# Optimization experiments

Measured on AMD Instinct MI355X. Metric: run time of the kernel, lower is better.

## Reference

```python
import jax, jax.numpy as jnp
import numpy as np

T, S, B, H, E, I = 64, 400, 32, 512, 1024, 128


def setup_inputs() -> dict:
    key = jax.random.key(0)
    ks = jax.random.split(key, 16)
    def n(k, shape, scale=1.0):
        return jax.random.normal(k, shape, dtype=jnp.float32) * scale
    return {
        "embedded_y": n(ks[0], (T, B, I)),
        "encode_outputs": n(ks[1], (S, B, E)),
        "init_state": n(ks[2], (B, H)),
        "x_mask": jnp.ones((S, B, 1), jnp.float32),
        "y_mask": jnp.ones((T, B, 1), jnp.float32),
        "x_index": jax.random.randint(ks[3], (S, B), 0, 50000, dtype=jnp.int32),
        "init_coverage": jnp.zeros((B, S), jnp.float32),
        # attention params
        "W_h": n(ks[4], (E, E), E ** -0.5),
        "W_s": n(ks[5], (E, H), H ** -0.5),
        "W_c": n(ks[6], (E, 1), 1.0),
        "b_attn": n(ks[7], (E,), 0.02),
        "V": n(ks[8], (1, E), E ** -0.5),
        # gru1: input I -> hidden H (torch gate order r, z, n)
        "w_ih1": n(ks[9], (3 * H, I), I ** -0.5),
        "w_hh1": n(ks[10], (3 * H, H), H ** -0.5),
        "b_ih1": jnp.zeros((3 * H,), jnp.float32),
        "b_hh1": jnp.zeros((3 * H,), jnp.float32),
        # gru2: input E(=2H) -> hidden H
        "w_ih2": n(ks[11], (3 * H, E), E ** -0.5),
        "w_hh2": n(ks[12], (3 * H, H), H ** -0.5),
        "b_ih2": jnp.zeros((3 * H,), jnp.float32),
        "b_hh2": jnp.zeros((3 * H,), jnp.float32),
    }


def _gru_cell(x, h, w_ih, w_hh, b_ih, b_hh):
    # single-step nn.GRU (torch gate order: r, z, n)
    gi = x @ w_ih.T + b_ih
    gh = h @ w_hh.T + b_hh
    i_r, i_z, i_n = jnp.split(gi, 3, axis=-1)
    h_r, h_z, h_n = jnp.split(gh, 3, axis=-1)
    r = jax.nn.sigmoid(i_r + h_r)
    z = jax.nn.sigmoid(i_z + h_z)
    n_ = jnp.tanh(i_n + r * h_n)
    return (1.0 - z) * n_ + z * h


def reference(embedded_y, encode_outputs, init_state, x_mask, y_mask, x_index,
              init_coverage, W_h, W_s, W_c, b_attn, V,
              w_ih1, w_hh1, b_ih1, b_hh1, w_ih2, w_hh2, b_ih2, b_hh2):
    # hoist the encoder projection out of the time loop (loop-invariant)
    Wh_enc = jnp.einsum('sbe,fe->sbf', encode_outputs, W_h)  # [S,B,E]
    wc = W_c[:, 0]  # [E], since W_c: Linear(1, E)

    def step(carry, inp):
        hidden, cov = carry          # [B,H], [B,S]
        y_t, ym = inp                # [B,I], [B,1]
        s1 = _gru_cell(y_t, hidden, w_ih1, w_hh1, b_ih1, b_hh1)
        s1 = ym * s1 + (1.0 - ym) * hidden
        # Bahdanau attention with coverage
        states = Wh_enc + (s1 @ W_s.T)[None, :, :] + cov.T[:, :, None] * wc + b_attn  # [S,B,E]
        score = (jnp.tanh(states) * x_mask) @ V.T            # [S,B,1]
        score = jnp.where(x_mask == 0, -1e9, score)
        aw = jax.nn.softmax(score, axis=0)                   # softmax over source positions
        ctx = jnp.sum(aw * encode_outputs, axis=0)           # [B,E]
        s2 = _gru_cell(ctx, s1, w_ih2, w_hh2, b_ih2, b_hh2)
        s2 = ym * s2 + (1.0 - ym) * s1
        wa = aw[:, :, 0].T                                   # [B,S]
        return (s2, cov + wa), (s2, ctx, wa, cov)

    _, (hidden_states, context_vectors, words_attention_weights, coverage_vectors) = \
        jax.lax.scan(step, (init_state, init_coverage), (embedded_y, y_mask))
    Tn = embedded_y.shape[0]
    x_index_t = x_index.T  # [B,S]
    x_indexes = jnp.broadcast_to(x_index_t[None], (Tn,) + x_index_t.shape)
    # is_predicting=False: coverage BEFORE each step (coverage_vectors_all[:-1])
    return (hidden_states, context_vectors, words_attention_weights, x_indexes, coverage_vectors)
```

## Files before the change

kernel.cpp:

```cpp
#include <hip/hip_runtime.h>
#include <cstdint>
#include <cstddef>

#define T_ 64
#define S_ 400
#define B_ 32
#define H_ 512
#define E_ 1024
#define I_ 128

__device__ __forceinline__ float sigmoid_(float x){ return 1.0f/(1.0f + __expf(-x)); }
__device__ __forceinline__ float tanh_(float x){
    float e = __expf(2.0f*fabsf(x));
    float t = 1.0f - 2.0f/(e + 1.0f);
    return copysignf(t, x);
}


__global__ __launch_bounds__(256) void init_kernel(const float* __restrict__ init_state,
        const float* __restrict__ init_cov, float* __restrict__ h0, float* __restrict__ cov){
    int i = blockIdx.x*256 + threadIdx.x;
    if (i < B_*H_) h0[i] = init_state[i];
    if (i < B_*S_) cov[i] = init_cov[i];
}

__global__ __launch_bounds__(256) void xidx_kernel(const int* __restrict__ x_index, float* __restrict__ out){
    int i = blockIdx.x*256 + threadIdx.x;
    if (i >= T_*B_*S_) return;
    int s = i % S_;
    int b = (i / S_) % B_;
    out[i] = (float)x_index[s*B_ + b];
}

#define BM 64
#define BN 64
#define BK 16
__global__ __launch_bounds__(256) void gemm_whenc(const float* __restrict__ A,
        const float* __restrict__ Bw, float* __restrict__ C){
    __shared__ float As[BK][BM];
    __shared__ float Bs[BK][BN];
    int bm = blockIdx.x;
    int bn = blockIdx.y;
    int tid = threadIdx.x;
    int lrow  = tid >> 2;
    int lcol4 = (tid & 3) * 4;
    int tx = tid & 15, ty = tid >> 4;
    const float* Ab = A  + (size_t)(bm*BM)*1024;
    const float* Bb = Bw + (size_t)(bn*BN)*1024;
    float acc[4][4] = {};
    for (int k0 = 0; k0 < 1024; k0 += BK){
        float4 av = *(const float4*)(Ab + (size_t)lrow*1024 + k0 + lcol4);
        float4 bv = *(const float4*)(Bb + (size_t)lrow*1024 + k0 + lcol4);
        As[lcol4+0][lrow]=av.x; As[lcol4+1][lrow]=av.y; As[lcol4+2][lrow]=av.z; As[lcol4+3][lrow]=av.w;
        Bs[lcol4+0][lrow]=bv.x; Bs[lcol4+1][lrow]=bv.y; Bs[lcol4+2][lrow]=bv.z; Bs[lcol4+3][lrow]=bv.w;
        __syncthreads();
        #pragma unroll
        for (int kk = 0; kk < BK; ++kk){
            float4 a4 = *(const float4*)&As[kk][ty*4];
            float4 b4 = *(const float4*)&Bs[kk][tx*4];
            float a_[4] = {a4.x, a4.y, a4.z, a4.w};
            float b_[4] = {b4.x, b4.y, b4.z, b4.w};
            #pragma unroll
            for (int i=0;i<4;++i)
                #pragma unroll
                for (int j=0;j<4;++j) acc[i][j] = fmaf(a_[i], b_[j], acc[i][j]);
        }
        __syncthreads();
    }
    int m0 = bm*BM + ty*4, n0 = bn*BN + tx*4;
    #pragma unroll
    for (int i=0;i<4;++i){
        float4 o = make_float4(acc[i][0], acc[i][1], acc[i][2], acc[i][3]);
        *(float4*)&C[(size_t)(m0+i)*E_ + n0] = o;
    }
}


__global__ __launch_bounds__(256) void gru1_kernel(const float* __restrict__ y,
        const float* __restrict__ hid,
        const float* __restrict__ w_ih, const float* __restrict__ w_hh,
        const float* __restrict__ b_ih, const float* __restrict__ b_hh,
        const float* __restrict__ ymask, float* __restrict__ s1, int t){
    __shared__ float xs[I_];
    __shared__ float hs[H_];
    __shared__ float part[3][64][6];
    int tid = threadIdx.x;
    int b = blockIdx.y;
    int hh = tid & 63, p = tid >> 6;
    int h = blockIdx.x*64 + hh;
    for (int i=tid; i<I_; i+=256) xs[i] = y[(size_t)t*B_*I_ + (size_t)b*I_ + i];
    for (int i=tid; i<H_; i+=256) hs[i] = hid[(size_t)b*H_ + i];
    __syncthreads();
    float gp[6];
    #pragma unroll
    for (int g=0; g<3; ++g){
        const float* wr = w_ih + (size_t)(g*H_ + h)*I_;
        float acc = 0.0f;
        for (int k = p*32; k < p*32 + 32; k += 4){
            float4 w4 = *(const float4*)(wr + k);
            acc = fmaf(w4.x, xs[k+0], acc); acc = fmaf(w4.y, xs[k+1], acc);
            acc = fmaf(w4.z, xs[k+2], acc); acc = fmaf(w4.w, xs[k+3], acc);
        }
        gp[g] = acc;
    }
    #pragma unroll
    for (int g=0; g<3; ++g){
        const float* wr = w_hh + (size_t)(g*H_ + h)*H_;
        float acc = 0.0f;
        for (int k = p*128; k < p*128 + 128; k += 4){
            float4 w4 = *(const float4*)(wr + k);
            acc = fmaf(w4.x, hs[k+0], acc); acc = fmaf(w4.y, hs[k+1], acc);
            acc = fmaf(w4.z, hs[k+2], acc); acc = fmaf(w4.w, hs[k+3], acc);
        }
        gp[3+g] = acc;
    }
    if (p){ 
        #pragma unroll
        for (int j=0;j<6;++j) part[p-1][hh][j] = gp[j]; 
    }
    __syncthreads();
    if (p == 0){
        float gi[3], gh[3];
        #pragma unroll
        for (int j=0;j<3;++j) gi[j] = gp[j]   + part[0][hh][j]   + part[1][hh][j]   + part[2][hh][j]   + b_ih[j*H_ + h];
        #pragma unroll
        for (int j=0;j<3;++j) gh[j] = gp[3+j] + part[0][hh][3+j] + part[1][hh][3+j] + part[2][hh][3+j] + b_hh[j*H_ + h];
        float r = sigmoid_(gi[0] + gh[0]);
        float z = sigmoid_(gi[1] + gh[1]);
        float n = tanh_(gi[2] + r*gh[2]);
        float hv = hs[h];
        float sv = (1.0f - z)*n + z*hv;
        float ym = ymask[t*B_ + b];
        s1[(size_t)b*H_ + h] = ym*sv + (1.0f - ym)*hv;
    }
}

__global__ __launch_bounds__(256) void qproj_kernel(const float* __restrict__ s1,
        const float* __restrict__ W_s, const float* __restrict__ b_attn, float* __restrict__ qb){
    __shared__ float hs[H_];
    __shared__ float part[3][64];
    int tid = threadIdx.x;
    int b = blockIdx.y;
    int ff = tid & 63, p = tid >> 6;
    int f = blockIdx.x*64 + ff;
    for (int i=tid; i<H_; i+=256) hs[i] = s1[(size_t)b*H_ + i];
    __syncthreads();
    const float* wr = W_s + (size_t)f*H_;
    float acc = 0.0f;
    for (int k = p*128; k < p*128 + 128; k += 4){
        float4 w4 = *(const float4*)(wr + k);
        acc = fmaf(w4.x, hs[k+0], acc); acc = fmaf(w4.y, hs[k+1], acc);
        acc = fmaf(w4.z, hs[k+2], acc); acc = fmaf(w4.w, hs[k+3], acc);
    }
    if (p) part[p-1][ff] = acc;
    __syncthreads();
    if (p == 0) qb[(size_t)b*E_ + f] = acc + part[0][ff] + part[1][ff] + part[2][ff] + b_attn[f];
}

__global__ __launch_bounds__(256) void score_kernel(const float* __restrict__ whenc,
        const float* __restrict__ qb, const float* __restrict__ cov,
        const float* __restrict__ wc, const float* __restrict__ Vv,
        const float* __restrict__ xmask, float* __restrict__ scores_t){
    int wave = blockIdx.x*4 + (threadIdx.x >> 6);
    int lane = threadIdx.x & 63;
    int s = wave >> 5, b = wave & 31;
    const float* wp = whenc + (size_t)(s*B_ + b)*E_;
    const float* qp = qb + (size_t)b*E_;
    float cv = cov[b*S_ + s];
    float acc = 0.0f;
    #pragma unroll
    for (int i=0;i<4;++i){
        int e = (i*64 + lane)*4;
        float4 w4 = *(const float4*)(wp + e);
        float4 q4 = *(const float4*)(qp + e);
        float4 c4 = *(const float4*)(wc + e);
        float4 v4 = *(const float4*)(Vv + e);
        acc = fmaf(v4.x, tanh_(w4.x + q4.x + cv*c4.x), acc);
        acc = fmaf(v4.y, tanh_(w4.y + q4.y + cv*c4.y), acc);
        acc = fmaf(v4.z, tanh_(w4.z + q4.z + cv*c4.z), acc);
        acc = fmaf(v4.w, tanh_(w4.w + q4.w + cv*c4.w), acc);
    }
    #pragma unroll
    for (int off=32; off; off>>=1) acc += __shfl_xor(acc, off);
    if (lane == 0){
        float xm = xmask[s*B_ + b];
        scores_t[b*S_ + s] = (xm == 0.0f) ? -1e9f : acc*xm;
    }
}

__global__ __launch_bounds__(256) void ctx_kernel(const float* __restrict__ scores_t,
        const float* __restrict__ enc, float* __restrict__ cov, float* __restrict__ ctxbuf,
        float* __restrict__ out_ctx, float* __restrict__ out_wa, float* __restrict__ out_cov, int t){
    __shared__ float p[S_];
    __shared__ float sacc[4][64];
    __shared__ float red[8];
    int tid = threadIdx.x;
    int b  = blockIdx.y;
    int e0 = blockIdx.x * 64;
    float v0 = scores_t[b*S_ + tid];
    float v1 = (tid + 256 < S_) ? scores_t[b*S_ + tid + 256] : -1e30f;
    float mx = fmaxf(v0, v1);
    #pragma unroll
    for (int off=32; off; off>>=1) mx = fmaxf(mx, __shfl_xor(mx, off));
    int wid = tid >> 6, lane = tid & 63;
    if (lane == 0) red[wid] = mx;
    __syncthreads();
    mx = fmaxf(fmaxf(red[0], red[1]), fmaxf(red[2], red[3]));
    float e0v = __expf(v0 - mx);
    float e1v = (tid + 256 < S_) ? __expf(v1 - mx) : 0.0f;
    float sm = e0v + e1v;
    #pragma unroll
    for (int off=32; off; off>>=1) sm += __shfl_xor(sm, off);
    if (lane == 0) red[4 + wid] = sm;
    __syncthreads();
    float rden = 1.0f/(red[4] + red[5] + red[6] + red[7]);
    p[tid] = e0v * rden;
    if (tid + 256 < S_) p[tid + 256] = e1v * rden;
    __syncthreads();
    const float* ep = enc + (size_t)b*E_ + e0 + lane;
    float acc = 0.0f;
    int sbeg = wid*100, send = sbeg + 100;
    #pragma unroll 4
    for (int s = sbeg; s < send; ++s)
        acc = fmaf(p[s], ep[(size_t)s*(B_*E_)], acc);
    sacc[wid][lane] = acc;
    __syncthreads();
    if (wid == 0){
        float a = sacc[0][lane] + sacc[1][lane] + sacc[2][lane] + sacc[3][lane];
        int e = e0 + lane;
        ctxbuf[(size_t)b*E_ + e] = a;
        out_ctx[(size_t)t*B_*E_ + (size_t)b*E_ + e] = a;
    }
    if (blockIdx.x == 0){
        for (int s = tid; s < S_; s += 256){
            float c = cov[b*S_ + s];
            out_wa [(size_t)t*B_*S_ + (size_t)b*S_ + s] = p[s];
            out_cov[(size_t)t*B_*S_ + (size_t)b*S_ + s] = c;
            cov[b*S_ + s] = c + p[s];
        }
    }
}

__global__ __launch_bounds__(256) void gru2_kernel(const float* __restrict__ ctx,
        const float* __restrict__ s1,
        const float* __restrict__ w_ih, const float* __restrict__ w_hh,
        const float* __restrict__ b_ih, const float* __restrict__ b_hh,
        const float* __restrict__ ymask, float* __restrict__ hnext,
        float* __restrict__ out_hidden, int t){
    __shared__ float xs[E_];
    __shared__ float hs[H_];
    __shared__ float part[3][64][6];
    int tid = threadIdx.x;
    int b = blockIdx.y;
    int hh = tid & 63, p = tid >> 6;
    int h = blockIdx.x*64 + hh;
    for (int i=tid; i<E_; i+=256) xs[i] = ctx[(size_t)b*E_ + i];
    for (int i=tid; i<H_; i+=256) hs[i] = s1[(size_t)b*H_ + i];
    __syncthreads();
    float gp[6];
    #pragma unroll
    for (int g=0; g<3; ++g){
        const float* wr = w_ih + (size_t)(g*H_ + h)*E_;
        float acc = 0.0f;
        for (int k = p*256; k < p*256 + 256; k += 4){
            float4 w4 = *(const float4*)(wr + k);
            acc = fmaf(w4.x, xs[k+0], acc); acc = fmaf(w4.y, xs[k+1], acc);
            acc = fmaf(w4.z, xs[k+2], acc); acc = fmaf(w4.w, xs[k+3], acc);
        }
        gp[g] = acc;
    }
    #pragma unroll
    for (int g=0; g<3; ++g){
        const float* wr = w_hh + (size_t)(g*H_ + h)*H_;
        float acc = 0.0f;
        for (int k = p*128; k < p*128 + 128; k += 4){
            float4 w4 = *(const float4*)(wr + k);
            acc = fmaf(w4.x, hs[k+0], acc); acc = fmaf(w4.y, hs[k+1], acc);
            acc = fmaf(w4.z, hs[k+2], acc); acc = fmaf(w4.w, hs[k+3], acc);
        }
        gp[3+g] = acc;
    }
    if (p){ 
        #pragma unroll
        for (int j=0;j<6;++j) part[p-1][hh][j] = gp[j]; 
    }
    __syncthreads();
    if (p == 0){
        float gi[3], gh[3];
        #pragma unroll
        for (int j=0;j<3;++j) gi[j] = gp[j]   + part[0][hh][j]   + part[1][hh][j]   + part[2][hh][j]   + b_ih[j*H_ + h];
        #pragma unroll
        for (int j=0;j<3;++j) gh[j] = gp[3+j] + part[0][hh][3+j] + part[1][hh][3+j] + part[2][hh][3+j] + b_hh[j*H_ + h];
        float r = sigmoid_(gi[0] + gh[0]);
        float z = sigmoid_(gi[1] + gh[1]);
        float n = tanh_(gi[2] + r*gh[2]);
        float s1v = hs[h];
        float sv = (1.0f - z)*n + z*s1v;
        float ym = ymask[t*B_ + b];
        float o = ym*sv + (1.0f - ym)*s1v;
        hnext[(size_t)b*H_ + h] = o;
        out_hidden[(size_t)t*B_*H_ + (size_t)b*H_ + h] = o;
    }
}


extern "C" void kernel_launch(void* const* d_in, const int* in_sizes, int n_in,
                              void* d_out, int out_size, void* d_ws, size_t ws_size,
                              hipStream_t stream) {
    const float* y          = (const float*)d_in[0];
    const float* enc        = (const float*)d_in[1];
    const float* init_state = (const float*)d_in[2];
    const float* xmask      = (const float*)d_in[3];
    const float* ymask      = (const float*)d_in[4];
    const int*   x_index    = (const int*)  d_in[5];
    const float* init_cov   = (const float*)d_in[6];
    const float* W_h        = (const float*)d_in[7];
    const float* W_s        = (const float*)d_in[8];
    const float* W_c        = (const float*)d_in[9];
    const float* b_attn     = (const float*)d_in[10];
    const float* Vv         = (const float*)d_in[11];
    const float* w_ih1      = (const float*)d_in[12];
    const float* w_hh1      = (const float*)d_in[13];
    const float* b_ih1      = (const float*)d_in[14];
    const float* b_hh1      = (const float*)d_in[15];
    const float* w_ih2      = (const float*)d_in[16];
    const float* w_hh2      = (const float*)d_in[17];
    const float* b_ih2      = (const float*)d_in[18];
    const float* b_hh2      = (const float*)d_in[19];

    float* out        = (float*)d_out;
    float* out_hidden = out;
    float* out_ctx    = out_hidden + (size_t)T_*B_*H_;
    float* out_wa     = out_ctx    + (size_t)T_*B_*E_;
    float* out_xidx   = out_wa     + (size_t)T_*B_*S_;
    float* out_cov    = out_xidx   + (size_t)T_*B_*S_;

    float* ws     = (float*)d_ws;
    float* whenc  = ws;
    float* qb     = whenc  + (size_t)S_*B_*E_;
    float* s1     = qb     + (size_t)B_*E_;
    float* h0     = s1     + (size_t)B_*H_;
    float* h1     = h0     + (size_t)B_*H_;
    float* cov    = h1     + (size_t)B_*H_;
    float* scores = cov    + (size_t)B_*S_;
    float* ctxbuf = scores + (size_t)B_*S_;

    init_kernel<<<64, 256, 0, stream>>>(init_state, init_cov, h0, cov);
    xidx_kernel<<<3200, 256, 0, stream>>>(x_index, out_xidx);
    gemm_whenc<<<dim3(200, 16), 256, 0, stream>>>(enc, W_h, whenc);

    for (int t = 0; t < T_; ++t){
        float* hcur  = (t & 1) ? h1 : h0;
        float* hnext = (t & 1) ? h0 : h1;
        gru1_kernel<<<dim3(8, 32), 256, 0, stream>>>(y, hcur, w_ih1, w_hh1, b_ih1, b_hh1, ymask, s1, t);
        qproj_kernel<<<dim3(16, 32), 256, 0, stream>>>(s1, W_s, b_attn, qb);
        score_kernel<<<3200, 256, 0, stream>>>(whenc, qb, cov, W_c, Vv, xmask, scores);
        ctx_kernel<<<dim3(16, 32), 256, 0, stream>>>(scores, enc, cov, ctxbuf, out_ctx, out_wa, out_cov, t);
        gru2_kernel<<<dim3(8, 32), 256, 0, stream>>>(ctxbuf, s1, w_ih2, w_hh2, b_ih2, b_hh2, ymask, hnext, out_hidden, t);
    }
}
```

Measured before the change: 7.281 ms.

## Fuse per-timestep decoder kernels into one persistent cooperative kernel with grid syncs

Replaces the five per-timestep kernel launches (gru1, qproj, score, ctx, gru2) with one cooperative persistent kernel of 256 blocks that loops over all timesteps and separates phases with grid.sync. Each block keeps its slice of the recurrent weights, W_s rows, W_c and V in LDS across timesteps. The goal is to remove launch overhead and repeated weight reloads. The trade-off is one block per CU, which leaves the bandwidth-heavy score and context phases at low occupancy, plus five grid-wide barriers per step.

```diff
diff --git a/kernel.cpp b/kernel.cpp
--- a/kernel.cpp
+++ b/kernel.cpp
@@ -1,6 +1,9 @@
 #include <hip/hip_runtime.h>
+#include <hip/hip_cooperative_groups.h>
 #include <cstdint>
 #include <cstddef>
+
+namespace cg = cooperative_groups;
 
 #define T_ 64
 #define S_ 400
@@ -15,13 +18,17 @@
     float t = 1.0f - 2.0f/(e + 1.0f);
     return copysignf(t, x);
 }
+__device__ __forceinline__ void fma4_(float& acc, float4 a, float4 b){
+    acc = fmaf(a.x,b.x,acc); acc = fmaf(a.y,b.y,acc);
+    acc = fmaf(a.z,b.z,acc); acc = fmaf(a.w,b.w,acc);
+}
 
 
 __global__ __launch_bounds__(256) void init_kernel(const float* __restrict__ init_state,
-        const float* __restrict__ init_cov, float* __restrict__ h0, float* __restrict__ cov){
+        const float* __restrict__ init_cov, float* __restrict__ h_g, float* __restrict__ covg){
     int i = blockIdx.x*256 + threadIdx.x;
-    if (i < B_*H_) h0[i] = init_state[i];
-    if (i < B_*S_) cov[i] = init_cov[i];
+    if (i < B_*H_) h_g[i] = init_state[i];
+    if (i < B_*S_) covg[i] = init_cov[i];
 }
 
 __global__ __launch_bounds__(256) void xidx_kernel(const int* __restrict__ x_index, float* __restrict__ out){
@@ -76,230 +83,239 @@
 }
 
 
-__global__ __launch_bounds__(256) void gru1_kernel(const float* __restrict__ y,
-        const float* __restrict__ hid,
-        const float* __restrict__ w_ih, const float* __restrict__ w_hh,
+struct PArgs {
+    const float *y, *enc, *xmask, *ymask, *whenc;
+    const float *w_ih1, *w_hh1, *b_ih1, *b_hh1;
+    const float *w_ih2, *w_hh2, *b_ih2, *b_hh2;
+    const float *W_s, *b_attn, *W_c, *V;
+    float *s1g, *qbg, *h_g, *covg, *scoresg;
+    float *out_hidden, *out_ctx, *out_wa, *out_cov;
+};
+
+template<int XDIM, bool WIH_LDS>
+__device__ __forceinline__ void gru_phase(int bid, int tid, int t,
+        const float* __restrict__ xsrc,
+        const float* __restrict__ hsrc,
+        const float* __restrict__ wih,
+        const float* __restrict__ whh_l,
         const float* __restrict__ b_ih, const float* __restrict__ b_hh,
-        const float* __restrict__ ymask, float* __restrict__ s1, int t){
-    __shared__ float xs[I_];
-    __shared__ float hs[H_];
-    __shared__ float part[3][64][6];
-    int tid = threadIdx.x;
-    int b = blockIdx.y;
-    int hh = tid & 63, p = tid >> 6;
-    int h = blockIdx.x*64 + hh;
-    for (int i=tid; i<I_; i+=256) xs[i] = y[(size_t)t*B_*I_ + (size_t)b*I_ + i];
-    for (int i=tid; i<H_; i+=256) hs[i] = hid[(size_t)b*H_ + i];
-    __syncthreads();
-    float gp[6];
+        const float* __restrict__ ymask,
+        float* __restrict__ dest, float* __restrict__ dest2)
+{
+    constexpr int XSEG = XDIM/8;
+    int b = tid >> 3, seg = tid & 7;
+    const float* xb = xsrc + (size_t)b*XDIM + seg*XSEG;
+    const float* hb = hsrc + (size_t)b*H_ + seg*64;
+    float acc[12];
+    #pragma unroll
+    for (int j=0;j<12;++j) acc[j]=0.f;
     #pragma unroll
     for (int g=0; g<3; ++g){
-        const float* wr = w_ih + (size_t)(g*H_ + h)*I_;
-        float acc = 0.0f;
-        for (int k = p*32; k < p*32 + 32; k += 4){
-            float4 w4 = *(const float4*)(wr + k);
-            acc = fmaf(w4.x, xs[k+0], acc); acc = fmaf(w4.y, xs[k+1], acc);
-            acc = fmaf(w4.z, xs[k+2], acc); acc = fmaf(w4.w, xs[k+3], acc);
-        }
-        gp[g] = acc;
+        const float* wr0;
+        const float* wr1;
+        if (WIH_LDS){
+            wr0 = wih + (g*2+0)*XDIM + seg*XSEG;
+            wr1 = wih + (g*2+1)*XDIM + seg*XSEG;
+        } else {
+            wr0 = wih + (size_t)(g*H_ + 2*bid + 0)*XDIM + seg*XSEG;
+            wr1 = wih + (size_t)(g*H_ + 2*bid + 1)*XDIM + seg*XSEG;
+        }
+        #pragma unroll 4
+        for (int k=0; k<XSEG; k+=4){
+            float4 xv = *(const float4*)(xb + k);
+            fma4_(acc[g*2+0], xv, *(const float4*)(wr0 + k));
+            fma4_(acc[g*2+1], xv, *(const float4*)(wr1 + k));
+        }
+        const float* hr0 = whh_l + (g*2+0)*H_ + seg*64;
+        const float* hr1 = whh_l + (g*2+1)*H_ + seg*64;
+        #pragma unroll 4
+        for (int k=0; k<64; k+=4){
+            float4 hv = *(const float4*)(hb + k);
+            fma4_(acc[6+g*2+0], hv, *(const float4*)(hr0 + k));
+            fma4_(acc[6+g*2+1], hv, *(const float4*)(hr1 + k));
+        }
     }
     #pragma unroll
-    for (int g=0; g<3; ++g){
-        const float* wr = w_hh + (size_t)(g*H_ + h)*H_;
-        float acc = 0.0f;
-        for (int k = p*128; k < p*128 + 128; k += 4){
-            float4 w4 = *(const float4*)(wr + k);
-            acc = fmaf(w4.x, hs[k+0], acc); acc = fmaf(w4.y, hs[k+1], acc);
-            acc = fmaf(w4.z, hs[k+2], acc); acc = fmaf(w4.w, hs[k+3], acc);
-        }
-        gp[3+g] = acc;
-    }
-    if (p){ 
+    for (int j=0;j<12;++j){
+        acc[j] += __shfl_xor(acc[j], 1);
+        acc[j] += __shfl_xor(acc[j], 2);
+        acc[j] += __shfl_xor(acc[j], 4);
+    }
+    if (seg == 0){
+        float ym = ymask[t*B_ + b];
         #pragma unroll
-        for (int j=0;j<6;++j) part[p-1][hh][j] = gp[j]; 
+        for (int hh=0; hh<2; ++hh){
+            int h = 2*bid + hh;
+            float gi_r = acc[0+hh] + b_ih[0*H_ + h];
+            float gi_z = acc[2+hh] + b_ih[1*H_ + h];
+            float gi_n = acc[4+hh] + b_ih[2*H_ + h];
+            float gh_r = acc[6+0+hh] + b_hh[0*H_ + h];
+            float gh_z = acc[6+2+hh] + b_hh[1*H_ + h];
+            float gh_n = acc[6+4+hh] + b_hh[2*H_ + h];
+            float r = sigmoid_(gi_r + gh_r);
+            float z = sigmoid_(gi_z + gh_z);
+            float n = tanh_(gi_n + r*gh_n);
+            float hv = hsrc[(size_t)b*H_ + h];
+            float o = ym*((1.f - z)*n + z*hv) + (1.f - ym)*hv;
+            dest[(size_t)b*H_ + h] = o;
+            if (dest2) dest2[(size_t)b*H_ + h] = o;
+        }
+    }
+}
+
+__global__ __launch_bounds__(256, 1) void decoder_persistent(PArgs a){
+    cg::grid_group grid = cg::this_grid();
+    extern __shared__ float smem[];
+    float* wih1_l = smem;
+    float* whh1_l = wih1_l + 6*I_;
+    float* whh2_l = whh1_l + 6*H_;
+    float* wsr    = whh2_l + 6*H_;
+    float* wc_l   = wsr + 4*H_;
+    float* v_l    = wc_l + E_;
+    float* ps     = v_l + E_;
+    float* tmp    = ps + S_;
+    float* red    = tmp + 128;
+
+    const int tid = threadIdx.x;
+    const int bid = blockIdx.x;
+
+    for (int i = tid; i < 6*I_; i += 256){
+        int j = i >> 7, k = i & (I_-1);
+        int g = j >> 1, hh = j & 1;
+        wih1_l[i] = a.w_ih1[(size_t)(g*H_ + 2*bid + hh)*I_ + k];
+    }
+    for (int i = tid; i < 6*H_; i += 256){
+        int j = i >> 9, k = i & (H_-1);
+        int g = j >> 1, hh = j & 1;
+        whh1_l[i] = a.w_hh1[(size_t)(g*H_ + 2*bid + hh)*H_ + k];
+        whh2_l[i] = a.w_hh2[(size_t)(g*H_ + 2*bid + hh)*H_ + k];
+    }
+    for (int i = tid; i < 4*H_; i += 256){
+        int j = i >> 9, k = i & (H_-1);
+        wsr[i] = a.W_s[(size_t)(4*bid + j)*H_ + k];
+    }
+    for (int i = tid; i < E_; i += 256){
+        wc_l[i] = a.W_c[i];
+        v_l[i]  = a.V[i];
     }
     __syncthreads();
-    if (p == 0){
-        float gi[3], gh[3];
-        #pragma unroll
-        for (int j=0;j<3;++j) gi[j] = gp[j]   + part[0][hh][j]   + part[1][hh][j]   + part[2][hh][j]   + b_ih[j*H_ + h];
-        #pragma unroll
-        for (int j=0;j<3;++j) gh[j] = gp[3+j] + part[0][hh][3+j] + part[1][hh][3+j] + part[2][hh][3+j] + b_hh[j*H_ + h];
-        float r = sigmoid_(gi[0] + gh[0]);
-        float z = sigmoid_(gi[1] + gh[1]);
-        float n = tanh_(gi[2] + r*gh[2]);
-        float hv = hs[h];
-        float sv = (1.0f - z)*n + z*hv;
-        float ym = ymask[t*B_ + b];
-        s1[(size_t)b*H_ + h] = ym*sv + (1.0f - ym)*hv;
-    }
-}
-
-__global__ __launch_bounds__(256) void qproj_kernel(const float* __restrict__ s1,
-        const float* __restrict__ W_s, const float* __restrict__ b_attn, float* __restrict__ qb){
-    __shared__ float hs[H_];
-    __shared__ float part[3][64];
-    int tid = threadIdx.x;
-    int b = blockIdx.y;
-    int ff = tid & 63, p = tid >> 6;
-    int f = blockIdx.x*64 + ff;
-    for (int i=tid; i<H_; i+=256) hs[i] = s1[(size_t)b*H_ + i];
-    __syncthreads();
-    const float* wr = W_s + (size_t)f*H_;
-    float acc = 0.0f;
-    for (int k = p*128; k < p*128 + 128; k += 4){
-        float4 w4 = *(const float4*)(wr + k);
-        acc = fmaf(w4.x, hs[k+0], acc); acc = fmaf(w4.y, hs[k+1], acc);
-        acc = fmaf(w4.z, hs[k+2], acc); acc = fmaf(w4.w, hs[k+3], acc);
-    }
-    if (p) part[p-1][ff] = acc;
-    __syncthreads();
-    if (p == 0) qb[(size_t)b*E_ + f] = acc + part[0][ff] + part[1][ff] + part[2][ff] + b_attn[f];
-}
-
-__global__ __launch_bounds__(256) void score_kernel(const float* __restrict__ whenc,
-        const float* __restrict__ qb, const float* __restrict__ cov,
-        const float* __restrict__ wc, const float* __restrict__ Vv,
-        const float* __restrict__ xmask, float* __restrict__ scores_t){
-    int wave = blockIdx.x*4 + (threadIdx.x >> 6);
-    int lane = threadIdx.x & 63;
-    int s = wave >> 5, b = wave & 31;
-    const float* wp = whenc + (size_t)(s*B_ + b)*E_;
-    const float* qp = qb + (size_t)b*E_;
-    float cv = cov[b*S_ + s];
-    float acc = 0.0f;
-    #pragma unroll
-    for (int i=0;i<4;++i){
-        int e = (i*64 + lane)*4;
-        float4 w4 = *(const float4*)(wp + e);
-        float4 q4 = *(const float4*)(qp + e);
-        float4 c4 = *(const float4*)(wc + e);
-        float4 v4 = *(const float4*)(Vv + e);
-        acc = fmaf(v4.x, tanh_(w4.x + q4.x + cv*c4.x), acc);
-        acc = fmaf(v4.y, tanh_(w4.y + q4.y + cv*c4.y), acc);
-        acc = fmaf(v4.z, tanh_(w4.z + q4.z + cv*c4.z), acc);
-        acc = fmaf(v4.w, tanh_(w4.w + q4.w + cv*c4.w), acc);
-    }
-    #pragma unroll
-    for (int off=32; off; off>>=1) acc += __shfl_xor(acc, off);
-    if (lane == 0){
-        float xm = xmask[s*B_ + b];
-        scores_t[b*S_ + s] = (xm == 0.0f) ? -1e9f : acc*xm;
-    }
-}
-
-__global__ __launch_bounds__(256) void ctx_kernel(const float* __restrict__ scores_t,
-        const float* __restrict__ enc, float* __restrict__ cov, float* __restrict__ ctxbuf,
-        float* __restrict__ out_ctx, float* __restrict__ out_wa, float* __restrict__ out_cov, int t){
-    __shared__ float p[S_];
-    __shared__ float sacc[4][64];
-    __shared__ float red[8];
-    int tid = threadIdx.x;
-    int b  = blockIdx.y;
-    int e0 = blockIdx.x * 64;
-    float v0 = scores_t[b*S_ + tid];
-    float v1 = (tid + 256 < S_) ? scores_t[b*S_ + tid + 256] : -1e30f;
-    float mx = fmaxf(v0, v1);
-    #pragma unroll
-    for (int off=32; off; off>>=1) mx = fmaxf(mx, __shfl_xor(mx, off));
-    int wid = tid >> 6, lane = tid & 63;
-    if (lane == 0) red[wid] = mx;
-    __syncthreads();
-    mx = fmaxf(fmaxf(red[0], red[1]), fmaxf(red[2], red[3]));
-    float e0v = __expf(v0 - mx);
-    float e1v = (tid + 256 < S_) ? __expf(v1 - mx) : 0.0f;
-    float sm = e0v + e1v;
-    #pragma unroll
-    for (int off=32; off; off>>=1) sm += __shfl_xor(sm, off);
-    if (lane == 0) red[4 + wid] = sm;
-    __syncthreads();
-    float rden = 1.0f/(red[4] + red[5] + red[6] + red[7]);
-    p[tid] = e0v * rden;
-    if (tid + 256 < S_) p[tid + 256] = e1v * rden;
-    __syncthreads();
-    const float* ep = enc + (size_t)b*E_ + e0 + lane;
-    float acc = 0.0f;
-    int sbeg = wid*100, send = sbeg + 100;
-    #pragma unroll 4
-    for (int s = sbeg; s < send; ++s)
-        acc = fmaf(p[s], ep[(size_t)s*(B_*E_)], acc);
-    sacc[wid][lane] = acc;
-    __syncthreads();
-    if (wid == 0){
-        float a = sacc[0][lane] + sacc[1][lane] + sacc[2][lane] + sacc[3][lane];
-        int e = e0 + lane;
-        ctxbuf[(size_t)b*E_ + e] = a;
-        out_ctx[(size_t)t*B_*E_ + (size_t)b*E_ + e] = a;
-    }
-    if (blockIdx.x == 0){
-        for (int s = tid; s < S_; s += 256){
-            float c = cov[b*S_ + s];
-            out_wa [(size_t)t*B_*S_ + (size_t)b*S_ + s] = p[s];
-            out_cov[(size_t)t*B_*S_ + (size_t)b*S_ + s] = c;
-            cov[b*S_ + s] = c + p[s];
-        }
-    }
-}
-
-__global__ __launch_bounds__(256) void gru2_kernel(const float* __restrict__ ctx,
-        const float* __restrict__ s1,
-        const float* __restrict__ w_ih, const float* __restrict__ w_hh,
-        const float* __restrict__ b_ih, const float* __restrict__ b_hh,
-        const float* __restrict__ ymask, float* __restrict__ hnext,
-        float* __restrict__ out_hidden, int t){
-    __shared__ float xs[E_];
-    __shared__ float hs[H_];
-    __shared__ float part[3][64][6];
-    int tid = threadIdx.x;
-    int b = blockIdx.y;
-    int hh = tid & 63, p = tid >> 6;
-    int h = blockIdx.x*64 + hh;
-    for (int i=tid; i<E_; i+=256) xs[i] = ctx[(size_t)b*E_ + i];
-    for (int i=tid; i<H_; i+=256) hs[i] = s1[(size_t)b*H_ + i];
-    __syncthreads();
-    float gp[6];
-    #pragma unroll
-    for (int g=0; g<3; ++g){
-        const float* wr = w_ih + (size_t)(g*H_ + h)*E_;
-        float acc = 0.0f;
-        for (int k = p*256; k < p*256 + 256; k += 4){
-            float4 w4 = *(const float4*)(wr + k);
-            acc = fmaf(w4.x, xs[k+0], acc); acc = fmaf(w4.y, xs[k+1], acc);
-            acc = fmaf(w4.z, xs[k+2], acc); acc = fmaf(w4.w, xs[k+3], acc);
-        }
-        gp[g] = acc;
-    }
-    #pragma unroll
-    for (int g=0; g<3; ++g){
-        const float* wr = w_hh + (size_t)(g*H_ + h)*H_;
-        float acc = 0.0f;
-        for (int k = p*128; k < p*128 + 128; k += 4){
-            float4 w4 = *(const float4*)(wr + k);
-            acc = fmaf(w4.x, hs[k+0], acc); acc = fmaf(w4.y, hs[k+1], acc);
-            acc = fmaf(w4.z, hs[k+2], acc); acc = fmaf(w4.w, hs[k+3], acc);
-        }
-        gp[3+g] = acc;
-    }
-    if (p){ 
-        #pragma unroll
-        for (int j=0;j<6;++j) part[p-1][hh][j] = gp[j]; 
-    }
-    __syncthreads();
-    if (p == 0){
-        float gi[3], gh[3];
-        #pragma unroll
-        for (int j=0;j<3;++j) gi[j] = gp[j]   + part[0][hh][j]   + part[1][hh][j]   + part[2][hh][j]   + b_ih[j*H_ + h];
-        #pragma unroll
-        for (int j=0;j<3;++j) gh[j] = gp[3+j] + part[0][hh][3+j] + part[1][hh][3+j] + part[2][hh][3+j] + b_hh[j*H_ + h];
-        float r = sigmoid_(gi[0] + gh[0]);
-        float z = sigmoid_(gi[1] + gh[1]);
-        float n = tanh_(gi[2] + r*gh[2]);
-        float s1v = hs[h];
-        float sv = (1.0f - z)*n + z*s1v;
-        float ym = ymask[t*B_ + b];
-        float o = ym*sv + (1.0f - ym)*s1v;
-        hnext[(size_t)b*H_ + h] = o;
-        out_hidden[(size_t)t*B_*H_ + (size_t)b*H_ + h] = o;
+
+    for (int t = 0; t < T_; ++t){
+        gru_phase<I_, true>(bid, tid, t, a.y + (size_t)t*B_*I_, a.h_g,
+                            wih1_l, whh1_l, a.b_ih1, a.b_hh1, a.ymask, a.s1g, nullptr);
+        grid.sync();
+
+        {
+            int b = tid >> 3, seg = tid & 7;
+            const float* sb = a.s1g + (size_t)b*H_ + seg*64;
+            float acc[4] = {0.f,0.f,0.f,0.f};
+            #pragma unroll 4
+            for (int k=0;k<64;k+=4){
+                float4 sv = *(const float4*)(sb + k);
+                #pragma unroll
+                for (int j=0;j<4;++j)
+                    fma4_(acc[j], sv, *(const float4*)(wsr + j*H_ + seg*64 + k));
+            }
+            #pragma unroll
+            for (int j=0;j<4;++j){
+                acc[j] += __shfl_xor(acc[j],1);
+                acc[j] += __shfl_xor(acc[j],2);
+                acc[j] += __shfl_xor(acc[j],4);
+            }
+            if (seg == 0){
+                #pragma unroll
+                for (int j=0;j<4;++j){
+                    int f = 4*bid + j;
+                    a.qbg[(size_t)b*E_ + f] = acc[j] + a.b_attn[f];
+                }
+            }
+        }
+        grid.sync();
+
+        {
+            int wid = tid >> 6, lane = tid & 63;
+            int base = bid*50;
+            #pragma unroll 1
+            for (int i = 0; i < 13; ++i){
+                int pi = base + wid + 4*i;
+                if (pi >= base + 50) break;
+                int s = pi >> 5, b = pi & 31;
+                const float* wp = a.whenc + (size_t)pi*E_;
+                const float* qp = a.qbg + (size_t)b*E_;
+                float cv = a.covg[b*S_ + s];
+                float acc = 0.f;
+                #pragma unroll
+                for (int pass=0; pass<4; ++pass){
+                    int e = pass*256 + lane*4;
+                    float4 w4 = *(const float4*)(wp + e);
+                    float4 q4 = *(const float4*)(qp + e);
+                    float4 c4 = *(const float4*)(wc_l + e);
+                    float4 v4 = *(const float4*)(v_l + e);
+                    acc = fmaf(v4.x, tanh_(w4.x + q4.x + cv*c4.x), acc);
+                    acc = fmaf(v4.y, tanh_(w4.y + q4.y + cv*c4.y), acc);
+                    acc = fmaf(v4.z, tanh_(w4.z + q4.z + cv*c4.z), acc);
+                    acc = fmaf(v4.w, tanh_(w4.w + q4.w + cv*c4.w), acc);
+                }
+                #pragma unroll
+                for (int off=32; off; off>>=1) acc += __shfl_xor(acc, off);
+                if (lane == 0){
+                    float xm = a.xmask[s*B_ + b];
+                    a.scoresg[b*S_ + s] = (xm == 0.f) ? -1e9f : acc*xm;
+                }
+            }
+        }
+        grid.sync();
+
+        {
+            int b = bid >> 3, e0 = (bid & 7)*128;
+            float v0g = a.scoresg[b*S_ + tid];
+            float v1g = (tid+256 < S_) ? a.scoresg[b*S_ + tid + 256] : -1e30f;
+            float mx = fmaxf(v0g, v1g);
+            #pragma unroll
+            for (int off=32; off; off>>=1) mx = fmaxf(mx, __shfl_xor(mx, off));
+            int wid = tid >> 6, lane = tid & 63;
+            if (lane == 0) red[wid] = mx;
+            __syncthreads();
+            mx = fmaxf(fmaxf(red[0],red[1]), fmaxf(red[2],red[3]));
+            float e0v = __expf(v0g - mx);
+            float e1v = (tid+256 < S_) ? __expf(v1g - mx) : 0.f;
+            float sm = e0v + e1v;
+            #pragma unroll
+            for (int off=32; off; off>>=1) sm += __shfl_xor(sm, off);
+            if (lane == 0) red[8+wid] = sm;
+            __syncthreads();
+            float rden = 1.f/(red[8]+red[9]+red[10]+red[11]);
+            ps[tid] = e0v*rden;
+            if (tid+256 < S_) ps[tid+256] = e1v*rden;
+            __syncthreads();
+            int sh = tid >> 7, eo = tid & 127;
+            const float* ep = a.enc + (size_t)b*E_ + e0 + eo;
+            float acc = 0.f;
+            int sbeg = sh*200;
+            #pragma unroll 4
+            for (int s = sbeg; s < sbeg+200; ++s)
+                acc = fmaf(ps[s], ep[(size_t)s*(B_*E_)], acc);
+            if (sh == 1) tmp[eo] = acc;
+            __syncthreads();
+            if (sh == 0){
+                float cv = acc + tmp[eo];
+                a.out_ctx[(size_t)t*B_*E_ + (size_t)b*E_ + e0 + eo] = cv;
+            }
+            if ((bid & 7) == 0){
+                for (int s = tid; s < S_; s += 256){
+                    float c = a.covg[b*S_ + s];
+                    a.out_wa [(size_t)t*B_*S_ + (size_t)b*S_ + s] = ps[s];
+                    a.out_cov[(size_t)t*B_*S_ + (size_t)b*S_ + s] = c;
+                    a.covg[b*S_ + s] = c + ps[s];
+                }
+            }
+        }
+        grid.sync();
+
+        gru_phase<E_, false>(bid, tid, t, a.out_ctx + (size_t)t*B_*E_, a.s1g,
+                             a.w_ih2, whh2_l, a.b_ih2, a.b_hh2, a.ymask, a.h_g,
+                             a.out_hidden + (size_t)t*B_*H_);
+        grid.sync();
     }
 }
 
@@ -335,27 +351,27 @@
     float* out_xidx   = out_wa     + (size_t)T_*B_*S_;
     float* out_cov    = out_xidx   + (size_t)T_*B_*S_;
 
-    float* ws     = (float*)d_ws;
-    float* whenc  = ws;
-    float* qb     = whenc  + (size_t)S_*B_*E_;
-    float* s1     = qb     + (size_t)B_*E_;
-    float* h0     = s1     + (size_t)B_*H_;
-    float* h1     = h0     + (size_t)B_*H_;
-    float* cov    = h1     + (size_t)B_*H_;
-    float* scores = cov    + (size_t)B_*S_;
-    float* ctxbuf = scores + (size_t)B_*S_;
-
-    init_kernel<<<64, 256, 0, stream>>>(init_state, init_cov, h0, cov);
+    float* ws      = (float*)d_ws;
+    float* whenc   = ws;
+    float* s1g     = whenc + (size_t)S_*B_*E_;
+    float* qbg     = s1g   + (size_t)B_*H_;
+    float* h_g     = qbg   + (size_t)B_*E_;
+    float* covg    = h_g   + (size_t)B_*H_;
+    float* scoresg = covg  + (size_t)B_*S_;
+
+    init_kernel<<<64, 256, 0, stream>>>(init_state, init_cov, h_g, covg);
     xidx_kernel<<<3200, 256, 0, stream>>>(x_index, out_xidx);
     gemm_whenc<<<dim3(200, 16), 256, 0, stream>>>(enc, W_h, whenc);
 
-    for (int t = 0; t < T_; ++t){
-        float* hcur  = (t & 1) ? h1 : h0;
-        float* hnext = (t & 1) ? h0 : h1;
-        gru1_kernel<<<dim3(8, 32), 256, 0, stream>>>(y, hcur, w_ih1, w_hh1, b_ih1, b_hh1, ymask, s1, t);
-        qproj_kernel<<<dim3(16, 32), 256, 0, stream>>>(s1, W_s, b_attn, qb);
-        score_kernel<<<3200, 256, 0, stream>>>(whenc, qb, cov, W_c, Vv, xmask, scores);
-        ctx_kernel<<<dim3(16, 32), 256, 0, stream>>>(scores, enc, cov, ctxbuf, out_ctx, out_wa, out_cov, t);
-        gru2_kernel<<<dim3(8, 32), 256, 0, stream>>>(ctxbuf, s1, w_ih2, w_hh2, b_ih2, b_hh2, ymask, hnext, out_hidden, t);
-    }
-}
+    PArgs pa;
+    pa.y = y; pa.enc = enc; pa.xmask = xmask; pa.ymask = ymask; pa.whenc = whenc;
+    pa.w_ih1 = w_ih1; pa.w_hh1 = w_hh1; pa.b_ih1 = b_ih1; pa.b_hh1 = b_hh1;
+    pa.w_ih2 = w_ih2; pa.w_hh2 = w_hh2; pa.b_ih2 = b_ih2; pa.b_hh2 = b_hh2;
+    pa.W_s = W_s; pa.b_attn = b_attn; pa.W_c = W_c; pa.V = Vv;
+    pa.s1g = s1g; pa.qbg = qbg; pa.h_g = h_g; pa.covg = covg; pa.scoresg = scoresg;
+    pa.out_hidden = out_hidden; pa.out_ctx = out_ctx; pa.out_wa = out_wa; pa.out_cov = out_cov;
+
+    void* args[] = { &pa };
+    hipLaunchCooperativeKernel((const void*)decoder_persistent, dim3(256), dim3(256),
+                               args, 46208, stream);
+}
```

Result: slower. 15.58 ms (+114.0%).
